# Kernel tuning notes

Measured on AMD Instinct MI355X. Metric: run time of the kernel, lower is better.

## Reference

```python
import jax, jax.numpy as jnp
import numpy as np

B, N, COUT, CIN, H, W = 16, 4, 256, 256, 64, 64


def setup_inputs() -> dict:
    key = jax.random.key(0)
    k1, k2, k3, k4 = jax.random.split(key, 4)
    x = jax.random.normal(k1, (B, CIN, H, W), jnp.float32)
    alphas = jax.random.uniform(k2, (B, N), jnp.float32)          # routing weights (lambdas)
    angles = jax.random.normal(k3, (B, N), jnp.float32) * 0.5     # thetas, mixed signs
    # kaiming_normal_(mode='fan_out', relu): std = sqrt(2 / (Cout * k * k))
    std = np.sqrt(2.0 / (COUT * 9)).astype(np.float32)
    weight = jax.random.normal(k4, (N, COUT, CIN, 3, 3), jnp.float32) * std
    return {"x": x, "alphas": alphas, "angles": angles, "weight": weight}


def _rot_mats(thetas):
    """thetas: [M] -> rotation matrices [M, 9, 9] (row, col), matching torch builder."""
    xc = jnp.cos(thetas)
    ys = jnp.sin(thetas)
    a = xc - ys
    b = xc * ys
    c = xc + ys
    z = jnp.zeros_like(xc)
    o = jnp.ones_like(xc)

    def mat(rows):
        # rows: list of 9 lists of 9 [M]-arrays -> [M, 9, 9]
        return jnp.stack([jnp.stack(r, axis=-1) for r in rows], axis=-2)

    pos = mat([
        [a, 1 - a, z, z, z, z, z, z, z],
        [z, xc - b, b, z, 1 - c + b, ys - b, z, z, z],
        [z, z, a, z, z, 1 - a, z, z, z],
        [b, ys - b, z, xc - b, 1 - c + b, z, z, z, z],
        [z, z, z, z, o, z, z, z, z],
        [z, z, z, z, 1 - c + b, xc - b, z, ys - b, b],
        [z, z, z, 1 - a, z, z, a, z, z],
        [z, z, z, ys - b, 1 - c + b, z, b, xc - b, z],
        [z, z, z, z, z, z, z, 1 - a, a],
    ])
    neg = mat([
        [c, z, z, 1 - c, z, z, z, z, z],
        [-b, xc + b, z, b - ys, 1 - a - b, z, z, z, z],
        [z, 1 - c, c, z, z, z, z, z, z],
        [z, z, z, xc + b, 1 - a - b, z, -b, b - ys, z],
        [z, z, z, z, o, z, z, z, z],
        [z, b - ys, -b, z, 1 - a - b, xc + b, z, z, z],
        [z, z, z, z, z, z, c, 1 - c, z],
        [z, z, z, z, 1 - a - b, b - ys, z, xc + b, -b],
        [z, z, z, z, z, 1 - c, z, z, c],
    ])
    m = (thetas >= 0).astype(thetas.dtype)[:, None, None]
    return m * pos + (1 - m) * neg


def reference(x, alphas, angles, weight):
    bsz, Cin, h, w = x.shape
    n, Cout = weight.shape[0], weight.shape[1]
    # [bsz, n, 9, 9] rotation matrices scaled by routing lambdas
    rm = _rot_mats(angles.reshape(-1)).reshape(bsz, n, 9, 9)
    rm = rm * alphas[:, :, None, None]
    # weights [n, Cout, Cin, 3, 3] -> [n, 9, Cout*Cin]
    Wf = weight.transpose(0, 3, 4, 1, 2).reshape(n, 9, Cout * Cin)
    # mix over kernel_number n and source tap q -> per-sample rotated kernels
    rw = jnp.einsum('bnpq,nqm->bpm', rm, Wf)          # [bsz, 9, Cout*Cin]
    rw = rw.reshape(bsz, 3, 3, Cout, Cin).transpose(0, 3, 4, 1, 2)
    rw = rw.reshape(bsz * Cout, Cin, 3, 3)
    # per-sample conv via grouped conv on flattened batch
    xr = x.reshape(1, bsz * Cin, h, w)
    out = jax.lax.conv_general_dilated(
        xr, rw, window_strides=(1, 1), padding=((1, 1), (1, 1)),
        dimension_numbers=('NCHW', 'OIHW', 'NCHW'), feature_group_count=bsz)
    return out.reshape(bsz, Cout, out.shape[2], out.shape[3])
```

## Files before the change

kernel.cpp:

```cpp
#include <hip/hip_runtime.h>
#include <hip/hip_bf16.h>

#define B_    16
#define N_    4
#define COUT  256
#define CIN   256
#define H_    64
#define W_    64
#define K_TOT (CIN * 9)
#define HW    (H_ * W_)
#define NKT   72
#define PAD   66
#define PLANE (PAD * PAD)

typedef __attribute__((ext_vector_type(8))) short short8;
typedef __attribute__((ext_vector_type(4))) float f32x4;
typedef unsigned short ushort_t;

static __device__ __forceinline__ ushort_t f2bf(float f) {
    __hip_bfloat16 h = __float2bfloat16(f);
    return *reinterpret_cast<ushort_t*>(&h);
}

typedef __attribute__((address_space(3))) unsigned int lds_u32;
typedef __attribute__((address_space(1))) const unsigned int glb_u32;
static __device__ __forceinline__ void gl_lds16(const ushort_t* g, ushort_t* l) {
    __builtin_amdgcn_global_load_lds((glb_u32*)g, (lds_u32*)l, 16, 0, 0);
}

#define BARRIER() asm volatile("s_barrier" ::: "memory")
#define VMCNTN(N) asm volatile("s_waitcnt vmcnt(" #N ")" ::: "memory")

__global__ void rot_mats_kernel(const float* __restrict__ alphas,
                                const float* __restrict__ angles,
                                float* __restrict__ rm) {
    int i = threadIdx.x;
    if (i >= B_ * N_) return;
    float th = angles[i], al = alphas[i];
    float xc = cosf(th), ys = sinf(th);
    float a = xc - ys, b = xc * ys, c = xc + ys;
    float r[81];
#pragma unroll
    for (int j = 0; j < 81; ++j) r[j] = 0.f;
    if (th >= 0.f) {
        r[0] = a;          r[1] = 1.f - a;
        r[10] = xc - b;    r[11] = b;        r[13] = 1.f - c + b; r[14] = ys - b;
        r[20] = a;         r[23] = 1.f - a;
        r[27] = b;         r[28] = ys - b;   r[30] = xc - b;      r[31] = 1.f - c + b;
        r[40] = 1.f;
        r[49] = 1.f - c + b; r[50] = xc - b; r[52] = ys - b;      r[53] = b;
        r[57] = 1.f - a;   r[60] = a;
        r[66] = ys - b;    r[67] = 1.f - c + b; r[69] = b;        r[70] = xc - b;
        r[79] = 1.f - a;   r[80] = a;
    } else {
        r[0] = c;          r[3] = 1.f - c;
        r[9] = -b;         r[10] = xc + b;   r[12] = b - ys;      r[13] = 1.f - a - b;
        r[19] = 1.f - c;   r[20] = c;
        r[30] = xc + b;    r[31] = 1.f - a - b; r[33] = -b;       r[34] = b - ys;
        r[40] = 1.f;
        r[46] = b - ys;    r[47] = -b;       r[49] = 1.f - a - b; r[50] = xc + b;
        r[60] = c;         r[61] = 1.f - c;
        r[67] = 1.f - a - b; r[68] = b - ys; r[70] = xc + b;      r[71] = -b;
        r[77] = 1.f - c;   r[80] = c;
    }
#pragma unroll
    for (int j = 0; j < 81; ++j) rm[i * 81 + j] = r[j] * al;
}

__global__ __launch_bounds__(256)
void build_rw_kernel(const float* __restrict__ weight,
                     const float* __restrict__ rm,
                     ushort_t* __restrict__ rw) {
    __shared__ float rms[N_ * 81];
    int tid = threadIdx.x;
    int b = blockIdx.y;
    for (int j = tid; j < N_ * 81; j += 256)
        rms[j] = rm[b * N_ * 81 + j];
    __syncthreads();

    int idx = blockIdx.x * 256 + tid;
    int cout = idx >> 8, cin = idx & 255;

    float wv[N_][9];
#pragma unroll
    for (int n = 0; n < N_; ++n)
#pragma unroll
        for (int q = 0; q < 9; ++q)
            wv[n][q] = weight[(size_t)(n * (COUT * CIN) + idx) * 9 + q];

    ushort_t* dst = rw + (size_t)(b * COUT + cout) * K_TOT + cin;
#pragma unroll
    for (int p = 0; p < 9; ++p) {
        float s = 0.f;
#pragma unroll
        for (int n = 0; n < N_; ++n)
#pragma unroll
            for (int q = 0; q < 9; ++q)
                s += rms[n * 81 + p * 9 + q] * wv[n][q];
        dst[p * 256] = f2bf(s);
    }
}

__global__ __launch_bounds__(256)
void halo_zero_kernel(ushort_t* __restrict__ xt) {
    ushort_t* base = xt + (size_t)blockIdx.x * PLANE * 64;
    int t = threadIdx.x;
    for (int i = t; i < 260; i += 256) {
        int py, px;
        if (i < 66)       { py = 0;  px = i; }
        else if (i < 132) { py = 65; px = i - 66; }
        else if (i < 196) { py = i - 132 + 1; px = 0; }
        else              { py = i - 196 + 1; px = 65; }
        ushort_t* d = base + (size_t)(py * PAD + px) * 64;
        int4 z = {0, 0, 0, 0};
#pragma unroll
        for (int q = 0; q < 8; ++q) *(int4*)(d + q * 8) = z;
    }
}

__global__ __launch_bounds__(256)
void nhwc_kernel(const float* __restrict__ x, ushort_t* __restrict__ xt) {
    int y    = blockIdx.x;
    int cb32 = blockIdx.y;
    int b    = blockIdx.z;
    __shared__ ushort_t tileT[64][40];
    int t = threadIdx.x;

    int ci = t & 31, seg = t >> 5;
    const float* src = x + ((size_t)(b * CIN + cb32 * 32 + ci) * HW + y * 64 + seg * 8);
    float4 f0 = ((const float4*)src)[0];
    float4 f1 = ((const float4*)src)[1];
#pragma unroll
    for (int q = 0; q < 4; ++q) tileT[seg * 8 + q][ci]     = f2bf(((float*)&f0)[q]);
#pragma unroll
    for (int q = 0; q < 4; ++q) tileT[seg * 8 + 4 + q][ci] = f2bf(((float*)&f1)[q]);
    __syncthreads();

    int px = t >> 2, cseg = t & 3;
    ushort_t* dst = xt + ((size_t)(b * 4 + (cb32 >> 1)) * PLANE + (y + 1) * PAD + px + 1) * 64
                       + (cb32 & 1) * 32 + cseg * 8;
    *(int4*)dst = *(const int4*)&tileT[px][cseg * 8];
}

__global__ __launch_bounds__(512, 1)
void conv_kernel(const ushort_t* __restrict__ xt,
                 const ushort_t* __restrict__ rw,
                 float* __restrict__ out) {
    int bid0 = blockIdx.x;
    int bid = (bid0 & 7) * 32 + (bid0 >> 3);
    int b     = bid >> 4;
    int ptile = bid & 15;
    int y0 = ptile * 4;
    int tid = threadIdx.x;
    int lane = tid & 63, wid = tid >> 6;
    int wm = wid >> 2, wn = wid & 3;
    int rA = lane & 15, kseg = lane >> 4;

    __shared__ __align__(16) ushort_t As[3][8192];
    __shared__ __align__(16) ushort_t Bs[3][8192];
    ushort_t* AsB = &As[0][0];
    ushort_t* BsB = &Bs[0][0];

    f32x4 acc[8][4] = {};

    const ushort_t* rwb = rw + (size_t)b * COUT * K_TOT;
    const ushort_t* xtb = xt + ((size_t)b * 4 * PLANE + (size_t)y0 * PAD) * 64;

    int asrc[2], bsrc[2], uDst[2];
#pragma unroll
    for (int i = 0; i < 2; ++i) {
        int u = i * 512 + tid;
        int l = u >> 3, s = u & 7;
        int c = s ^ (l & 7);
        int row = 2 * l + (c >> 2);
        asrc[i] = row * K_TOT + (c & 3) * 8;
        bsrc[i] = ((row >> 6) * PAD + (row & 63)) * 64 + (c & 3) * 8;
        uDst[i] = u * 8;
    }
    const int slotR = (kseg + 4 * (rA & 1)) ^ ((rA >> 1) & 7);
    const int aRd = (wm * 64 + (rA >> 1)) * 64 + slotR * 8;
    const int bRd = (wn * 32 + (rA >> 1)) * 64 + slotR * 8;

#define STAGE_AB(KT, Q)                                                        \
    {                                                                          \
        int p_ = (KT) >> 3, sub_ = (KT) & 7;                                   \
        int ako = p_ * 256 + sub_ * 32;                                        \
        gl_lds16(rwb + asrc[0] + ako, AsB + (Q) * 8192 + uDst[0]);             \
        gl_lds16(rwb + asrc[1] + ako, AsB + (Q) * 8192 + uDst[1]);             \
        int ph_ = p_ / 3, pw_ = p_ - 3 * ph_;                                  \
        const ushort_t* sb_ = xtb + (size_t)((sub_ >> 1) * PLANE + ph_ * PAD + pw_) * 64 \
                              + (sub_ & 1) * 32;                               \
        gl_lds16(sb_ + bsrc[0], BsB + (Q) * 8192 + uDst[0]);                   \
        gl_lds16(sb_ + bsrc[1], BsB + (Q) * 8192 + uDst[1]);                   \
    }

#define READ_FRAGS(Q, AF, BF)                                                  \
    _Pragma("unroll")                                                          \
    for (int mi = 0; mi < 8; ++mi)                                             \
        AF[mi] = *(const short8*)(AsB + (Q) * 8192 + aRd + mi * 512);          \
    _Pragma("unroll")                                                          \
    for (int ni = 0; ni < 4; ++ni)                                             \
        BF[ni] = *(const short8*)(BsB + (Q) * 8192 + bRd + ni * 512);

#define TILE_BODY(KT, QN, QS, AFC, BFC, AFN, BFN)                              \
    {                                                                          \
        if ((KT) + 1 < NKT) { READ_FRAGS(QN, AFN, BFN); }                      \
        if ((KT) + 2 < NKT) { STAGE_AB((KT) + 2, QS); }                        \
        __builtin_amdgcn_s_setprio(1);                                         \
        _Pragma("unroll")                                                      \
        for (int mi = 0; mi < 8; ++mi)                                         \
            _Pragma("unroll")                                                  \
            for (int ni = 0; ni < 4; ++ni)                                     \
                acc[mi][ni] = __builtin_amdgcn_mfma_f32_16x16x32_bf16(         \
                    AFC[mi], BFC[ni], acc[mi][ni], 0, 0, 0);                   \
        __builtin_amdgcn_s_setprio(0);                                         \
        VMCNTN(0);                                                             \
        BARRIER();                                                             \
    }

    STAGE_AB(0, 0);
    STAGE_AB(1, 1);
    VMCNTN(0);
    BARRIER();

    short8 afA[8], bfA[4], afB[8], bfB[4];
    READ_FRAGS(0, afA, bfA);

    int qc = 0;
    for (int kt = 0; kt < NKT; kt += 2) {
        int qn = qc + 1; if (qn >= 3) qn -= 3;
        int qs = qc + 2; if (qs >= 3) qs -= 3;
        TILE_BODY(kt, qn, qs, afA, bfA, afB, bfB);
        int qn2 = qs;
        int qs2 = qc;
        TILE_BODY(kt + 1, qn2, qs2, afB, bfB, afA, bfA);
        qc = qs;
    }
#undef TILE_BODY
#undef READ_FRAGS
#undef STAGE_AB

    int row0 = (lane >> 4) * 4;
    int col  = lane & 15;
    float* outb = out + (size_t)b * COUT * HW + ptile * 256;
#pragma unroll
    for (int am = 0; am < 8; ++am)
#pragma unroll
        for (int an = 0; an < 4; ++an)
#pragma unroll
            for (int rr = 0; rr < 4; ++rr) {
                int m = wm * 128 + am * 16 + row0 + rr;
                int n = wn * 64 + an * 16 + col;
                outb[(size_t)m * HW + n] = acc[am][an][rr];
            }
}

extern "C" void kernel_launch(void* const* d_in, const int* in_sizes, int n_in,
                              void* d_out, int out_size, void* d_ws, size_t ws_size,
                              hipStream_t stream) {
    const float* x      = (const float*)d_in[0];
    const float* alphas = (const float*)d_in[1];
    const float* angles = (const float*)d_in[2];
    const float* weight = (const float*)d_in[3];
    float* out = (float*)d_out;

    ushort_t* rw = (ushort_t*)d_ws;
    ushort_t* xt = (ushort_t*)((char*)d_ws + (size_t)B_ * COUT * K_TOT * 2);
    float*    rm = (float*)((char*)d_ws + (size_t)B_ * COUT * K_TOT * 2
                                        + (size_t)64 * PLANE * 64 * 2);

    rot_mats_kernel<<<1, 64, 0, stream>>>(alphas, angles, rm);
    build_rw_kernel<<<dim3(COUT * CIN / 256, B_), 256, 0, stream>>>(weight, rm, rw);
    halo_zero_kernel<<<64, 256, 0, stream>>>(xt);
    nhwc_kernel<<<dim3(64, 8, B_), 256, 0, stream>>>(x, xt);
    conv_kernel<<<256, 512, 0, stream>>>(xt, rw, out);
}
```

Measured before the change: 117.1 us.

## Fuse rotation-matrix and halo-zero kernels into weight build and NHWC transpose

Rotation-matrix construction moves into build_rw_kernel, where each block computes all 64 matrices into shared memory and loops over the batch. The weights are then read once per block instead of once per sample. Halo zeroing moves into nhwc_kernel, which removes two kernel launches. The cost is less parallelism in build_rw (256 blocks instead of 4096) and redundant matrix computation in every block.

```diff
diff --git a/kernel.cpp b/kernel.cpp
--- a/kernel.cpp
+++ b/kernel.cpp
@@ -31,51 +31,45 @@
 #define BARRIER() asm volatile("s_barrier" ::: "memory")
 #define VMCNTN(N) asm volatile("s_waitcnt vmcnt(" #N ")" ::: "memory")
 
-__global__ void rot_mats_kernel(const float* __restrict__ alphas,
-                                const float* __restrict__ angles,
-                                float* __restrict__ rm) {
-    int i = threadIdx.x;
-    if (i >= B_ * N_) return;
-    float th = angles[i], al = alphas[i];
-    float xc = cosf(th), ys = sinf(th);
-    float a = xc - ys, b = xc * ys, c = xc + ys;
-    float r[81];
-#pragma unroll
-    for (int j = 0; j < 81; ++j) r[j] = 0.f;
-    if (th >= 0.f) {
-        r[0] = a;          r[1] = 1.f - a;
-        r[10] = xc - b;    r[11] = b;        r[13] = 1.f - c + b; r[14] = ys - b;
-        r[20] = a;         r[23] = 1.f - a;
-        r[27] = b;         r[28] = ys - b;   r[30] = xc - b;      r[31] = 1.f - c + b;
-        r[40] = 1.f;
-        r[49] = 1.f - c + b; r[50] = xc - b; r[52] = ys - b;      r[53] = b;
-        r[57] = 1.f - a;   r[60] = a;
-        r[66] = ys - b;    r[67] = 1.f - c + b; r[69] = b;        r[70] = xc - b;
-        r[79] = 1.f - a;   r[80] = a;
-    } else {
-        r[0] = c;          r[3] = 1.f - c;
-        r[9] = -b;         r[10] = xc + b;   r[12] = b - ys;      r[13] = 1.f - a - b;
-        r[19] = 1.f - c;   r[20] = c;
-        r[30] = xc + b;    r[31] = 1.f - a - b; r[33] = -b;       r[34] = b - ys;
-        r[40] = 1.f;
-        r[46] = b - ys;    r[47] = -b;       r[49] = 1.f - a - b; r[50] = xc + b;
-        r[60] = c;         r[61] = 1.f - c;
-        r[67] = 1.f - a - b; r[68] = b - ys; r[70] = xc + b;      r[71] = -b;
-        r[77] = 1.f - c;   r[80] = c;
-    }
-#pragma unroll
-    for (int j = 0; j < 81; ++j) rm[i * 81 + j] = r[j] * al;
-}
-
 __global__ __launch_bounds__(256)
 void build_rw_kernel(const float* __restrict__ weight,
-                     const float* __restrict__ rm,
+                     const float* __restrict__ alphas,
+                     const float* __restrict__ angles,
                      ushort_t* __restrict__ rw) {
-    __shared__ float rms[N_ * 81];
+    __shared__ float rms[B_ * N_ * 81];
     int tid = threadIdx.x;
-    int b = blockIdx.y;
-    for (int j = tid; j < N_ * 81; j += 256)
-        rms[j] = rm[b * N_ * 81 + j];
+
+    if (tid < B_ * N_) {
+        float th = angles[tid], al = alphas[tid];
+        float xc = cosf(th), ys = sinf(th);
+        float a = xc - ys, b = xc * ys, c = xc + ys;
+        float r[81];
+#pragma unroll
+        for (int j = 0; j < 81; ++j) r[j] = 0.f;
+        if (th >= 0.f) {
+            r[0] = a;          r[1] = 1.f - a;
+            r[10] = xc - b;    r[11] = b;        r[13] = 1.f - c + b; r[14] = ys - b;
+            r[20] = a;         r[23] = 1.f - a;
+            r[27] = b;         r[28] = ys - b;   r[30] = xc - b;      r[31] = 1.f - c + b;
+            r[40] = 1.f;
+            r[49] = 1.f - c + b; r[50] = xc - b; r[52] = ys - b;      r[53] = b;
+            r[57] = 1.f - a;   r[60] = a;
+            r[66] = ys - b;    r[67] = 1.f - c + b; r[69] = b;        r[70] = xc - b;
+            r[79] = 1.f - a;   r[80] = a;
+        } else {
+            r[0] = c;          r[3] = 1.f - c;
+            r[9] = -b;         r[10] = xc + b;   r[12] = b - ys;      r[13] = 1.f - a - b;
+            r[19] = 1.f - c;   r[20] = c;
+            r[30] = xc + b;    r[31] = 1.f - a - b; r[33] = -b;       r[34] = b - ys;
+            r[40] = 1.f;
+            r[46] = b - ys;    r[47] = -b;       r[49] = 1.f - a - b; r[50] = xc + b;
+            r[60] = c;         r[61] = 1.f - c;
+            r[67] = 1.f - a - b; r[68] = b - ys; r[70] = xc + b;      r[71] = -b;
+            r[77] = 1.f - c;   r[80] = c;
+        }
+#pragma unroll
+        for (int j = 0; j < 81; ++j) rms[tid * 81 + j] = r[j] * al;
+    }
     __syncthreads();
 
     int idx = blockIdx.x * 256 + tid;
@@ -88,33 +82,19 @@
         for (int q = 0; q < 9; ++q)
             wv[n][q] = weight[(size_t)(n * (COUT * CIN) + idx) * 9 + q];
 
-    ushort_t* dst = rw + (size_t)(b * COUT + cout) * K_TOT + cin;
-#pragma unroll
-    for (int p = 0; p < 9; ++p) {
-        float s = 0.f;
-#pragma unroll
-        for (int n = 0; n < N_; ++n)
-#pragma unroll
-            for (int q = 0; q < 9; ++q)
-                s += rms[n * 81 + p * 9 + q] * wv[n][q];
-        dst[p * 256] = f2bf(s);
-    }
-}
-
-__global__ __launch_bounds__(256)
-void halo_zero_kernel(ushort_t* __restrict__ xt) {
-    ushort_t* base = xt + (size_t)blockIdx.x * PLANE * 64;
-    int t = threadIdx.x;
-    for (int i = t; i < 260; i += 256) {
-        int py, px;
-        if (i < 66)       { py = 0;  px = i; }
-        else if (i < 132) { py = 65; px = i - 66; }
-        else if (i < 196) { py = i - 132 + 1; px = 0; }
-        else              { py = i - 196 + 1; px = 65; }
-        ushort_t* d = base + (size_t)(py * PAD + px) * 64;
-        int4 z = {0, 0, 0, 0};
-#pragma unroll
-        for (int q = 0; q < 8; ++q) *(int4*)(d + q * 8) = z;
+    for (int b = 0; b < B_; ++b) {
+        const float* rmb = &rms[b * N_ * 81];
+        ushort_t* dst = rw + (size_t)(b * COUT + cout) * K_TOT + cin;
+#pragma unroll
+        for (int p = 0; p < 9; ++p) {
+            float s = 0.f;
+#pragma unroll
+            for (int n = 0; n < N_; ++n)
+#pragma unroll
+                for (int q = 0; q < 9; ++q)
+                    s += rmb[n * 81 + p * 9 + q] * wv[n][q];
+            dst[p * 256] = f2bf(s);
+        }
     }
 }
 
@@ -126,6 +106,9 @@
     __shared__ ushort_t tileT[64][40];
     int t = threadIdx.x;
 
+    ushort_t* plane = xt + (size_t)(b * 4 + (cb32 >> 1)) * PLANE * 64 + (cb32 & 1) * 32;
+    const int4 z = {0, 0, 0, 0};
+
     int ci = t & 31, seg = t >> 5;
     const float* src = x + ((size_t)(b * CIN + cb32 * 32 + ci) * HW + y * 64 + seg * 8);
     float4 f0 = ((const float4*)src)[0];
@@ -134,11 +117,24 @@
     for (int q = 0; q < 4; ++q) tileT[seg * 8 + q][ci]     = f2bf(((float*)&f0)[q]);
 #pragma unroll
     for (int q = 0; q < 4; ++q) tileT[seg * 8 + 4 + q][ci] = f2bf(((float*)&f1)[q]);
+
+    if (t < 8) {
+        int col = (t >> 2) ? 65 : 0;
+        int sg  = t & 3;
+        *(int4*)(plane + ((size_t)(y + 1) * PAD + col) * 64 + sg * 8) = z;
+    }
+    if (y == 0) {
+        for (int u = t; u < 528; u += 256) {
+            int row = (u >= 264) ? 65 : 0;
+            int v = (u >= 264) ? u - 264 : u;
+            int px = v >> 2, sg = v & 3;
+            *(int4*)(plane + ((size_t)row * PAD + px) * 64 + sg * 8) = z;
+        }
+    }
     __syncthreads();
 
     int px = t >> 2, cseg = t & 3;
-    ushort_t* dst = xt + ((size_t)(b * 4 + (cb32 >> 1)) * PLANE + (y + 1) * PAD + px + 1) * 64
-                       + (cb32 & 1) * 32 + cseg * 8;
+    ushort_t* dst = plane + ((size_t)(y + 1) * PAD + px + 1) * 64 + cseg * 8;
     *(int4*)dst = *(const int4*)&tileT[px][cseg * 8];
 }
 
@@ -266,12 +262,8 @@
 
     ushort_t* rw = (ushort_t*)d_ws;
     ushort_t* xt = (ushort_t*)((char*)d_ws + (size_t)B_ * COUT * K_TOT * 2);
-    float*    rm = (float*)((char*)d_ws + (size_t)B_ * COUT * K_TOT * 2
-                                        + (size_t)64 * PLANE * 64 * 2);
-
-    rot_mats_kernel<<<1, 64, 0, stream>>>(alphas, angles, rm);
-    build_rw_kernel<<<dim3(COUT * CIN / 256, B_), 256, 0, stream>>>(weight, rm, rw);
-    halo_zero_kernel<<<64, 256, 0, stream>>>(xt);
+
+    build_rw_kernel<<<COUT * CIN / 256, 256, 0, stream>>>(weight, alphas, angles, rw);
     nhwc_kernel<<<dim3(64, 8, B_), 256, 0, stream>>>(x, xt);
     conv_kernel<<<256, 512, 0, stream>>>(xt, rw, out);
 }
```

Measured after the change: 127.2 us. 1.09x slower.
